# Kernel optimization log

Measured on AMD Instinct MI355X. Metric: run time of the kernel, lower is better.

The kernel has to match this reference:

```python
import jax, jax.numpy as jnp
import numpy as np

NUM_EXPERTS = 8
HIDDEN = 2048
FFN = 1376
CAPACITY_FACTOR = 1.25
SCORE_SCALE = 1.0


def setup_inputs() -> dict:
    key = jax.random.key(0)
    k = jax.random.split(key, 6)
    T = 8192
    x = jax.random.normal(k[0], (T, HIDDEN), dtype=jnp.float32)
    topK_indices = jax.random.randint(k[1], (T,), 0, NUM_EXPERTS, dtype=jnp.int64)
    topK_scores = jax.random.uniform(k[2], (T,), dtype=jnp.float32)
    s = 1.0 / np.sqrt(HIDDEN)
    w_gate = jax.random.normal(k[3], (NUM_EXPERTS, HIDDEN, FFN), dtype=jnp.float32) * s
    w_up = jax.random.normal(k[4], (NUM_EXPERTS, HIDDEN, FFN), dtype=jnp.float32) * s
    w_down = jax.random.normal(k[5], (NUM_EXPERTS, FFN, HIDDEN), dtype=jnp.float32) * (1.0 / np.sqrt(FFN))
    return {"x": x, "topK_indices": topK_indices, "topK_scores": topK_scores,
            "w_gate": w_gate, "w_up": w_up, "w_down": w_down}


def reference(x, topK_indices, topK_scores, w_gate, w_up, w_down):
    T, D = x.shape
    E = w_gate.shape[0]
    capacity = int(CAPACITY_FACTOR * T / E)  # static (depends only on shapes)
    # position of each token within its assigned expert (deterministic drop:
    # keep the first `capacity` tokens in sequence order per expert)
    oh = jax.nn.one_hot(topK_indices, E, dtype=jnp.int32)          # [T,E]
    rank = jnp.take_along_axis(jnp.cumsum(oh, axis=0) - 1,
                               topK_indices[:, None].astype(jnp.int32), axis=1)[:, 0]
    keep = rank < capacity                                          # [T]
    # dispatch into per-expert capacity buffers; dropped tokens go to dummy slot
    slot = jnp.where(keep, topK_indices.astype(jnp.int32) * capacity + rank, E * capacity)
    buf = jnp.zeros((E * capacity + 1, D), x.dtype)
    buf = buf.at[slot].set(jnp.where(keep[:, None], x, jnp.zeros_like(x)))
    xe = buf[:E * capacity].reshape(E, capacity, D)                 # [E,C,D]
    # per-expert SwiGLU MLP as grouped GEMMs
    h = jax.nn.silu(jnp.einsum('ecd,edf->ecf', xe, w_gate)) * jnp.einsum('ecd,edf->ecf', xe, w_up)
    out = jnp.einsum('ecf,efd->ecd', h, w_down).reshape(E * capacity, D)
    out = jnp.concatenate([out, jnp.zeros((1, D), out.dtype)], axis=0)
    # combine: dropped tokens -> zero (dropped_padding='zero'), gate-score fusion
    y = out[slot] * keep[:, None].astype(out.dtype)
    y = y * (topK_scores[:, None] * SCORE_SCALE)
    return y
```

## Files before the change

kernel.cpp:

```cpp
#include <hip/hip_runtime.h>
#include <hip/hip_bf16.h>
#include <cstdint>
#include <cstddef>

#define NTOK 8192
#define DH   2048
#define DF   1376
#define DFP  1408
#define NE   8
#define CAP  1280

typedef __bf16 bf16x8 __attribute__((ext_vector_type(8)));
typedef float  f32x4  __attribute__((ext_vector_type(4)));

#define BARRIER() asm volatile("s_barrier" ::: "memory")
#define WAITV0()  asm volatile("s_waitcnt vmcnt(0)" ::: "memory")
#define WAITV6()  asm volatile("s_waitcnt vmcnt(6)" ::: "memory")
#define WAITV8()  asm volatile("s_waitcnt vmcnt(8)" ::: "memory")
#define SETPRIO(n) __builtin_amdgcn_s_setprio(n)

__device__ __forceinline__ uint32_t pk2(float a, float b) {
  float2 f; f.x = a; f.y = b;
  union { __hip_bfloat162 h; uint32_t u; } cv;
  cv.h = __float22bfloat162_rn(f);
  return cv.u;
}
__device__ __forceinline__ ushort bf16bits(float a) {
  return (ushort)(pk2(a, 0.f) & 0xFFFFu);
}
__device__ __forceinline__ void gload16(const ushort* g, ushort* l) {
  __builtin_amdgcn_global_load_lds(
      (const __attribute__((address_space(1))) uint32_t*)(const void*)g,
      (__attribute__((address_space(3))) uint32_t*)(void*)l,
      16, 0, 0);
}

__global__ void routing_kernel(const int* __restrict__ idx, int* __restrict__ tok_slot,
                               int* __restrict__ tok_keep) {
  __shared__ int cnt[256][NE];
  const int t = threadIdx.x;
  for (int s = t; s < NE * CAP; s += 256) tok_slot[s] = -1;
  unsigned long long cA = 0ull, cB = 0ull;
  const int per = NTOK / 256, base = t * per;
  for (int i = 0; i < per; ++i) {
    int e = idx[base + i];
    unsigned long long inc = 1ull << ((e & 3) * 16);
    if (e < 4) cA += inc; else cB += inc;
  }
#pragma unroll
  for (int e = 0; e < 4; ++e) cnt[t][e]     = (int)((cA >> (e * 16)) & 0xFFFF);
#pragma unroll
  for (int e = 0; e < 4; ++e) cnt[t][4 + e] = (int)((cB >> (e * 16)) & 0xFFFF);
  __syncthreads();
  if (t < NE) {
    int run = 0;
    for (int i = 0; i < 256; ++i) { int c = cnt[i][t]; cnt[i][t] = run; run += c; }
  }
  __syncthreads();
  cA = 0ull; cB = 0ull;
#pragma unroll
  for (int e = 0; e < 4; ++e) cA |= (unsigned long long)(cnt[t][e] & 0xFFFF) << (e * 16);
#pragma unroll
  for (int e = 0; e < 4; ++e) cB |= (unsigned long long)(cnt[t][4 + e] & 0xFFFF) << (e * 16);
  for (int i = 0; i < per; ++i) {
    int token = base + i;
    int e = idx[token];
    int sh = (e & 3) * 16;
    int r = (int)(((e < 4 ? cA : cB) >> sh) & 0xFFFF);
    unsigned long long inc = 1ull << sh;
    if (e < 4) cA += inc; else cB += inc;
    bool keep = (r < CAP);
    tok_keep[token] = keep ? 1 : 0;
    if (keep) tok_slot[e * CAP + r] = token;
  }
}

__global__ void zero_dropped(const int* __restrict__ keep, float* __restrict__ y) {
  if (keep[blockIdx.x]) return;
  float4 z = {0.f, 0.f, 0.f, 0.f};
  float* p = y + (size_t)blockIdx.x * DH + threadIdx.x * 8;
  *(float4*)p = z;
  *(float4*)(p + 4) = z;
}

__global__ void convert_x(const float* __restrict__ x, ushort* __restrict__ xb) {
  int i = (blockIdx.x * 256 + threadIdx.x) * 8;
  float4 a = *(const float4*)(x + i);
  float4 b = *(const float4*)(x + i + 4);
  uint4 p = { pk2(a.x, a.y), pk2(a.z, a.w), pk2(b.x, b.y), pk2(b.z, b.w) };
  *(uint4*)(xb + i) = p;
}

__global__ __launch_bounds__(256) void transpose_cvt(
    const float* __restrict__ in, ushort* __restrict__ out, int K, int N) {
  __shared__ ushort T[64][72];
  const int tid = threadIdx.x;
  const int n0 = blockIdx.x * 64, k0 = blockIdx.y * 64;
  const size_t eoff_in  = (size_t)blockIdx.z * K * N;
  const size_t eoff_out = (size_t)blockIdx.z * N * K;
  const int kr = tid >> 4;
  const int nc = (tid & 15) * 4;
#pragma unroll
  for (int it = 0; it < 4; ++it) {
    int k = k0 + kr + it * 16;
    int n = n0 + nc;
    float4 v = {0.f, 0.f, 0.f, 0.f};
    if (k < K && n + 4 <= N) v = *(const float4*)(in + eoff_in + (size_t)k * N + n);
    T[nc + 0][kr + it * 16] = bf16bits(v.x);
    T[nc + 1][kr + it * 16] = bf16bits(v.y);
    T[nc + 2][kr + it * 16] = bf16bits(v.z);
    T[nc + 3][kr + it * 16] = bf16bits(v.w);
  }
  __syncthreads();
  const int nr = tid >> 2;
  const int kc = tid & 3;
#pragma unroll
  for (int it = 0; it < 2; ++it) {
    int kloc = kc * 16 + it * 8;
    int n = n0 + nr, k = k0 + kloc;
    if (n < N && k + 8 <= K)
      *(uint4*)(out + eoff_out + (size_t)n * K + k) = *(const uint4*)&T[nr][kloc];
  }
}

__global__ void pad_h(ushort* __restrict__ h) {
  int idx = blockIdx.x * 512 + threadIdx.x;
  int row = idx >> 2, q = idx & 3;
  uint4 z = {0u, 0u, 0u, 0u};
  *(uint4*)(h + (size_t)row * DFP + DF + q * 8) = z;
}

__global__ __launch_bounds__(512, 1) void gemm_gateup3(
    const ushort* __restrict__ xb, const ushort* __restrict__ wgt,
    const ushort* __restrict__ wut, const int* __restrict__ tok_slot,
    ushort* __restrict__ h)
{
  __shared__ __align__(16) char sm[131072];
  const int tid = threadIdx.x, lane = tid & 63, wid = tid >> 6;
  const int wr = wid >> 1, wc = wid & 1;
  const int l15 = lane & 15, l4 = lane >> 4;

  int wgid = (blockIdx.x & 7) * 55 + (blockIdx.x >> 3);
  const int e = wgid / 55;
  const int rem = wgid - e * 55;
  const int mt = rem / 11, nt = rem - (rem / 11) * 11;
  const int n0 = nt * 128;

  const ushort* srcA[2]; const ushort* srcBg; const ushort* srcBu;
#pragma unroll
  for (int c = 0; c < 2; ++c) {
    int o = c * 8192 + wid * 1024 + lane * 16;
    int os = o ^ (((o >> 6) & 3) << 4);
    int row = os >> 6, kb = os & 63;
    int tk = tok_slot[e * CAP + mt * 256 + row];
    if (tk < 0) tk = 0;
    srcA[c] = xb + (size_t)tk * DH + (kb >> 1);
  }
  {
    int o = wid * 1024 + lane * 16;
    int os = o ^ (((o >> 6) & 3) << 4);
    int row = os >> 6, kb = os & 63;
    int n = n0 + row; if (n > DF - 1) n = DF - 1;
    srcBg = wgt + ((size_t)e * DF + n) * DH + (kb >> 1);
    srcBu = wut + ((size_t)e * DF + n) * DH + (kb >> 1);
  }
  int aoff[4], boff[4];
#pragma unroll
  for (int i = 0; i < 4; ++i) {
    int row = wr * 64 + i * 16 + l15;
    aoff[i] = row * 64 + ((l4 * 16) ^ ((l15 & 3) << 4));
  }
#pragma unroll
  for (int j = 0; j < 4; ++j) {
    int row = wc * 64 + j * 16 + l15;
    boff[j] = row * 64 + ((l4 * 16) ^ ((l15 & 3) << 4));
  }
  const int dstw = wid * 1024;

  f32x4 accG[4][4], accU[4][4];
#pragma unroll
  for (int i = 0; i < 4; ++i)
#pragma unroll
    for (int j = 0; j < 4; ++j) {
      accG[i][j] = (f32x4){0.f, 0.f, 0.f, 0.f};
      accU[i][j] = (f32x4){0.f, 0.f, 0.f, 0.f};
    }

  const int NT = DH / 32;
#pragma unroll
  for (int t0 = 0; t0 < 3; ++t0) {
    int kk = t0 * 32;
    gload16(srcA[0] + kk, (ushort*)(sm + t0 * 16384 + dstw));
    gload16(srcA[1] + kk, (ushort*)(sm + t0 * 16384 + 8192 + dstw));
    gload16(srcBg   + kk, (ushort*)(sm + 65536 + t0 * 8192 + dstw));
    gload16(srcBu   + kk, (ushort*)(sm + 98304 + t0 * 8192 + dstw));
  }
  WAITV8();
  BARRIER();

  for (int t = 0; t < NT; ++t) {
    const int r = t & 3, w = (t + 3) & 3;
    char* Ab  = sm + r * 16384;
    char* Bgb = sm + 65536 + r * 8192;
    char* Bub = sm + 98304 + r * 8192;
    bf16x8 a[4], bg[4], bu[4];
#pragma unroll
    for (int i = 0; i < 4; ++i) a[i]  = *(const bf16x8*)(Ab + aoff[i]);
#pragma unroll
    for (int j = 0; j < 4; ++j) bg[j] = *(const bf16x8*)(Bgb + boff[j]);
#pragma unroll
    for (int j = 0; j < 4; ++j) bu[j] = *(const bf16x8*)(Bub + boff[j]);
    if (t + 3 < NT) {
      int kk = (t + 3) * 32;
      gload16(srcA[0] + kk, (ushort*)(sm + w * 16384 + dstw));
      gload16(srcA[1] + kk, (ushort*)(sm + w * 16384 + 8192 + dstw));
      gload16(srcBg   + kk, (ushort*)(sm + 65536 + w * 8192 + dstw));
      gload16(srcBu   + kk, (ushort*)(sm + 98304 + w * 8192 + dstw));
    }
    SETPRIO(1);
#pragma unroll
    for (int j = 0; j < 4; ++j)
#pragma unroll
      for (int i = 0; i < 4; ++i)
        accG[i][j] = __builtin_amdgcn_mfma_f32_16x16x32_bf16(a[i], bg[j], accG[i][j], 0, 0, 0);
#pragma unroll
    for (int j = 0; j < 4; ++j)
#pragma unroll
      for (int i = 0; i < 4; ++i)
        accU[i][j] = __builtin_amdgcn_mfma_f32_16x16x32_bf16(a[i], bu[j], accU[i][j], 0, 0, 0);
    SETPRIO(0);
    if (t >= NT - 2) { WAITV0(); } else { WAITV8(); }
    BARRIER();
  }
  const size_t rowbase = (size_t)(e * CAP + mt * 256 + wr * 64);
#pragma unroll
  for (int j = 0; j < 4; ++j) {
    int col = n0 + wc * 64 + j * 16 + l15;
    if (col < DF) {
#pragma unroll
      for (int i = 0; i < 4; ++i)
#pragma unroll
        for (int r2 = 0; r2 < 4; ++r2) {
          size_t row = rowbase + i * 16 + l4 * 4 + r2;
          float gv = accG[i][j][r2], uv = accU[i][j][r2];
          h[row * DFP + col] = bf16bits(gv / (1.f + __expf(-gv)) * uv);
        }
    }
  }
}

__global__ __launch_bounds__(512, 1) void gemm_down3(
    const ushort* __restrict__ h, const ushort* __restrict__ wdt,
    const int* __restrict__ tok_slot, const float* __restrict__ scores,
    float* __restrict__ y)
{
  __shared__ __align__(16) char sm[149504];
  int* tokc = (int*)(sm + 147456);
  float* scc = (float*)(sm + 148480);
  const int tid = threadIdx.x, lane = tid & 63, wid = tid >> 6;
  const int wr = wid >> 1, wc = wid & 1;
  const int l15 = lane & 15, l4 = lane >> 4;

  int wgid = (blockIdx.x & 7) * 80 + (blockIdx.x >> 3);
  const int e = wgid / 80;
  const int rem = wgid - e * 80;
  const int mt = rem / 16, nt = rem & 15;
  const int n0 = nt * 128;

  if (tid < 256) {
    int tk = tok_slot[e * CAP + mt * 256 + tid];
    tokc[tid] = tk;
    scc[tid] = (tk >= 0) ? scores[tk] : 0.f;
  }
  __syncthreads();

  const size_t hrow0 = (size_t)(e * CAP + mt * 256);
  const ushort* srcA[4]; const ushort* srcB[2];
#pragma unroll
  for (int c = 0; c < 4; ++c) {
    int o = c * 8192 + wid * 1024 + lane * 16;
    int os = o ^ (((o >> 7) & 7) << 4);
    int row = os >> 7, kb = os & 127;
    srcA[c] = h + (hrow0 + row) * DFP + (kb >> 1);
  }
#pragma unroll
  for (int c = 0; c < 2; ++c) {
    int o = c * 8192 + wid * 1024 + lane * 16;
    int os = o ^ (((o >> 7) & 7) << 4);
    int row = os >> 7, kb = os & 127;
    srcB[c] = wdt + ((size_t)e * DH + n0 + row) * DF + (kb >> 1);
  }
  int aoff0[4], aoff1[4], boff0[4], boff1[4];
#pragma unroll
  for (int i = 0; i < 4; ++i) {
    int row = wr * 64 + i * 16 + l15;
    int r4 = (row & 7) << 4;
    aoff0[i] = row * 128 + ((l4 * 16) ^ r4);
    aoff1[i] = row * 128 + ((l4 * 16 + 64) ^ r4);
  }
#pragma unroll
  for (int j = 0; j < 4; ++j) {
    int row = wc * 64 + j * 16 + l15;
    int r4 = (row & 7) << 4;
    boff0[j] = row * 128 + ((l4 * 16) ^ r4);
    boff1[j] = row * 128 + ((l4 * 16 + 64) ^ r4);
  }
  const int dstw = wid * 1024;

  f32x4 acc[4][4];
#pragma unroll
  for (int i = 0; i < 4; ++i)
#pragma unroll
    for (int j = 0; j < 4; ++j) acc[i][j] = (f32x4){0.f, 0.f, 0.f, 0.f};

  const int NT = DFP / 64;
#pragma unroll
  for (int t0 = 0; t0 < 2; ++t0) {
    int kk = t0 * 64;
#pragma unroll
    for (int c = 0; c < 4; ++c)
      gload16(srcA[c] + kk, (ushort*)(sm + t0 * 32768 + c * 8192 + dstw));
#pragma unroll
    for (int c = 0; c < 2; ++c)
      gload16(srcB[c] + kk, (ushort*)(sm + 98304 + t0 * 16384 + c * 8192 + dstw));
  }
  WAITV6();
  BARRIER();

  int rrot = 0, wrot = 2;
  for (int t = 0; t < NT; ++t) {
    char* Ab = sm + rrot * 32768;
    char* Bb = sm + 98304 + rrot * 16384;
    bf16x8 a0[4], a1[4], b0[4], b1[4];
#pragma unroll
    for (int i = 0; i < 4; ++i) a0[i] = *(const bf16x8*)(Ab + aoff0[i]);
#pragma unroll
    for (int j = 0; j < 4; ++j) b0[j] = *(const bf16x8*)(Bb + boff0[j]);
#pragma unroll
    for (int i = 0; i < 4; ++i) a1[i] = *(const bf16x8*)(Ab + aoff1[i]);
#pragma unroll
    for (int j = 0; j < 4; ++j) b1[j] = *(const bf16x8*)(Bb + boff1[j]);
    if (t + 2 < NT) {
      int kk = (t + 2) * 64;
#pragma unroll
      for (int c = 0; c < 4; ++c)
        gload16(srcA[c] + kk, (ushort*)(sm + wrot * 32768 + c * 8192 + dstw));
#pragma unroll
      for (int c = 0; c < 2; ++c)
        gload16(srcB[c] + kk, (ushort*)(sm + 98304 + wrot * 16384 + c * 8192 + dstw));
    }
    SETPRIO(1);
#pragma unroll
    for (int j = 0; j < 4; ++j)
#pragma unroll
      for (int i = 0; i < 4; ++i)
        acc[i][j] = __builtin_amdgcn_mfma_f32_16x16x32_bf16(a0[i], b0[j], acc[i][j], 0, 0, 0);
#pragma unroll
    for (int j = 0; j < 4; ++j)
#pragma unroll
      for (int i = 0; i < 4; ++i)
        acc[i][j] = __builtin_amdgcn_mfma_f32_16x16x32_bf16(a1[i], b1[j], acc[i][j], 0, 0, 0);
    SETPRIO(0);
    if (t >= NT - 2) { WAITV0(); } else { WAITV6(); }
    BARRIER();
    rrot = (rrot == 2) ? 0 : rrot + 1;
    wrot = (wrot == 2) ? 0 : wrot + 1;
  }
  int tkr[4][4]; float sr[4][4];
#pragma unroll
  for (int i = 0; i < 4; ++i)
#pragma unroll
    for (int r = 0; r < 4; ++r) {
      int rl = wr * 64 + i * 16 + l4 * 4 + r;
      tkr[i][r] = tokc[rl];
      sr[i][r]  = scc[rl];
    }
#pragma unroll
  for (int j = 0; j < 4; ++j) {
    int col = n0 + wc * 64 + j * 16 + l15;
#pragma unroll
    for (int i = 0; i < 4; ++i)
#pragma unroll
      for (int r = 0; r < 4; ++r)
        if (tkr[i][r] >= 0)
          y[(size_t)tkr[i][r] * DH + col] = acc[i][j][r] * sr[i][r];
  }
}

extern "C" void kernel_launch(void* const* d_in, const int* in_sizes, int n_in,
                              void* d_out, int out_size, void* d_ws, size_t ws_size,
                              hipStream_t stream) {
  const float* x   = (const float*)d_in[0];
  const int*   idx = (const int*)d_in[1];
  const float* sc  = (const float*)d_in[2];
  const float* wg  = (const float*)d_in[3];
  const float* wu  = (const float*)d_in[4];
  const float* wd  = (const float*)d_in[5];
  float* y = (float*)d_out;

  const size_t OFF_KEEP = 40960;
  const size_t OFF_H    = 73728;
  const size_t SZ_H     = (size_t)NE * CAP * DFP * 2;
  const size_t OFF_XB   = OFF_H + SZ_H;
  const size_t SZ_XB    = (size_t)NTOK * DH * 2;
  const size_t OFF_WGT  = OFF_XB + SZ_XB;
  const size_t SZ_W     = (size_t)NE * DH * DF * 2;
  const size_t OFF_WUT  = OFF_WGT + SZ_W;

  int* tok_slot = (int*)d_ws;
  int* tok_keep = (int*)((char*)d_ws + OFF_KEEP);
  ushort* hbuf = (ushort*)((char*)d_ws + OFF_H);
  ushort* xb   = (ushort*)((char*)d_ws + OFF_XB);
  ushort* wgt  = (ushort*)((char*)d_ws + OFF_WGT);
  ushort* wut  = (ushort*)((char*)d_ws + OFF_WUT);
  ushort* wdt  = wgt;

  hipLaunchKernelGGL(routing_kernel, dim3(1), dim3(256), 0, stream, idx, tok_slot, tok_keep);
  hipLaunchKernelGGL(zero_dropped, dim3(NTOK), dim3(256), 0, stream, tok_keep, y);
  hipLaunchKernelGGL(convert_x, dim3(NTOK * DH / 2048), dim3(256), 0, stream, x, xb);
  hipLaunchKernelGGL(transpose_cvt, dim3((DF + 63) / 64, DH / 64, NE), dim3(256), 0, stream,
                     wg, wgt, DH, DF);
  hipLaunchKernelGGL(transpose_cvt, dim3((DF + 63) / 64, DH / 64, NE), dim3(256), 0, stream,
                     wu, wut, DH, DF);
  hipLaunchKernelGGL(pad_h, dim3(80), dim3(512), 0, stream, hbuf);
  hipLaunchKernelGGL(gemm_gateup3, dim3(440), dim3(512), 0, stream,
                     xb, wgt, wut, tok_slot, hbuf);
  hipLaunchKernelGGL(transpose_cvt, dim3(DH / 64, (DF + 63) / 64, NE), dim3(256), 0, stream,
                     wd, wdt, DF, DH);
  hipLaunchKernelGGL(gemm_down3, dim3(640), dim3(512), 0, stream,
                     hbuf, wdt, tok_slot, sc, y);
}
```

Baseline: 350.0 us.

## Use row-paired LDS swizzle and 4-stage K=32 pipeline in down GEMM

Both GEMMs switch to a new LDS layout that packs two 32-element K rows into each 128-byte line with an XOR swizzle, aimed at reducing LDS bank conflicts on the MFMA fragment reads. The down-projection kernel changes from a 3-buffer K=64 pipeline to a 4-buffer K=32 pipeline prefetching three tiles ahead, which shrinks its shared memory footprint. The vmcnt waits at the pipeline tail are graduated instead of draining everything early. Smaller K steps mean more barriers per unit of work in the down GEMM.

New measurement: 356.0 us. No clear change (+1.7%).

```diff
diff --git a/kernel.cpp b/kernel.cpp
--- a/kernel.cpp
+++ b/kernel.cpp
@@ -14,9 +14,7 @@
 typedef float  f32x4  __attribute__((ext_vector_type(4)));
 
 #define BARRIER() asm volatile("s_barrier" ::: "memory")
-#define WAITV0()  asm volatile("s_waitcnt vmcnt(0)" ::: "memory")
-#define WAITV6()  asm volatile("s_waitcnt vmcnt(6)" ::: "memory")
-#define WAITV8()  asm volatile("s_waitcnt vmcnt(8)" ::: "memory")
+#define WAITV(n)  asm volatile("s_waitcnt vmcnt(" #n ")" ::: "memory")
 #define SETPRIO(n) __builtin_amdgcn_s_setprio(n)
 
 __device__ __forceinline__ uint32_t pk2(float a, float b) {
@@ -33,6 +31,16 @@
       (const __attribute__((address_space(1))) uint32_t*)(const void*)g,
       (__attribute__((address_space(3))) uint32_t*)(void*)l,
       16, 0, 0);
+}
+
+__device__ __forceinline__ void rp_src(int o, int& row, int& ko) {
+  int p = o >> 7;
+  int g = ((o >> 4) & 7) ^ (p & 7);
+  row = p * 2 + (g >> 2);
+  ko  = (g & 3) * 8;
+}
+__device__ __forceinline__ int rp_off(int row, int l4) {
+  return ((row >> 1) << 7) + (((((row & 1) << 2) + l4) ^ ((row >> 1) & 7)) << 4);
 }
 
 __global__ void routing_kernel(const int* __restrict__ idx, int* __restrict__ tok_slot,
@@ -150,31 +158,23 @@
 #pragma unroll
   for (int c = 0; c < 2; ++c) {
     int o = c * 8192 + wid * 1024 + lane * 16;
-    int os = o ^ (((o >> 6) & 3) << 4);
-    int row = os >> 6, kb = os & 63;
+    int row, ko; rp_src(o, row, ko);
     int tk = tok_slot[e * CAP + mt * 256 + row];
     if (tk < 0) tk = 0;
-    srcA[c] = xb + (size_t)tk * DH + (kb >> 1);
+    srcA[c] = xb + (size_t)tk * DH + ko;
   }
   {
     int o = wid * 1024 + lane * 16;
-    int os = o ^ (((o >> 6) & 3) << 4);
-    int row = os >> 6, kb = os & 63;
+    int row, ko; rp_src(o, row, ko);
     int n = n0 + row; if (n > DF - 1) n = DF - 1;
-    srcBg = wgt + ((size_t)e * DF + n) * DH + (kb >> 1);
-    srcBu = wut + ((size_t)e * DF + n) * DH + (kb >> 1);
+    srcBg = wgt + ((size_t)e * DF + n) * DH + ko;
+    srcBu = wut + ((size_t)e * DF + n) * DH + ko;
   }
   int aoff[4], boff[4];
 #pragma unroll
-  for (int i = 0; i < 4; ++i) {
-    int row = wr * 64 + i * 16 + l15;
-    aoff[i] = row * 64 + ((l4 * 16) ^ ((l15 & 3) << 4));
-  }
-#pragma unroll
-  for (int j = 0; j < 4; ++j) {
-    int row = wc * 64 + j * 16 + l15;
-    boff[j] = row * 64 + ((l4 * 16) ^ ((l15 & 3) << 4));
-  }
+  for (int i = 0; i < 4; ++i) aoff[i] = rp_off(wr * 64 + i * 16 + l15, l4);
+#pragma unroll
+  for (int j = 0; j < 4; ++j) boff[j] = rp_off(wc * 64 + j * 16 + l15, l4);
   const int dstw = wid * 1024;
 
   f32x4 accG[4][4], accU[4][4];
@@ -195,7 +195,7 @@
     gload16(srcBg   + kk, (ushort*)(sm + 65536 + t0 * 8192 + dstw));
     gload16(srcBu   + kk, (ushort*)(sm + 98304 + t0 * 8192 + dstw));
   }
-  WAITV8();
+  WAITV(8);
   BARRIER();
 
   for (int t = 0; t < NT; ++t) {
@@ -229,7 +229,9 @@
       for (int i = 0; i < 4; ++i)
         accU[i][j] = __builtin_amdgcn_mfma_f32_16x16x32_bf16(a[i], bu[j], accU[i][j], 0, 0, 0);
     SETPRIO(0);
-    if (t >= NT - 2) { WAITV0(); } else { WAITV8(); }
+    if (t + 3 < NT)      { WAITV(8); }
+    else if (t + 2 < NT) { WAITV(4); }
+    else if (t + 1 < NT) { WAITV(0); }
     BARRIER();
   }
   const size_t rowbase = (size_t)(e * CAP + mt * 256 + wr * 64);
@@ -254,9 +256,9 @@
     const int* __restrict__ tok_slot, const float* __restrict__ scores,
     float* __restrict__ y)
 {
-  __shared__ __align__(16) char sm[149504];
-  int* tokc = (int*)(sm + 147456);
-  float* scc = (float*)(sm + 148480);
+  __shared__ __align__(16) char sm[100352];
+  int* tokc = (int*)(sm + 98304);
+  float* scc = (float*)(sm + 99328);
   const int tid = threadIdx.x, lane = tid & 63, wid = tid >> 6;
   const int wr = wid >> 1, wc = wid & 1;
   const int l15 = lane & 15, l4 = lane >> 4;
@@ -275,36 +277,23 @@
   __syncthreads();
 
   const size_t hrow0 = (size_t)(e * CAP + mt * 256);
-  const ushort* srcA[4]; const ushort* srcB[2];
-#pragma unroll
-  for (int c = 0; c < 4; ++c) {
-    int o = c * 8192 + wid * 1024 + lane * 16;
-    int os = o ^ (((o >> 7) & 7) << 4);
-    int row = os >> 7, kb = os & 127;
-    srcA[c] = h + (hrow0 + row) * DFP + (kb >> 1);
-  }
+  const ushort* srcA[2]; const ushort* srcB;
 #pragma unroll
   for (int c = 0; c < 2; ++c) {
     int o = c * 8192 + wid * 1024 + lane * 16;
-    int os = o ^ (((o >> 7) & 7) << 4);
-    int row = os >> 7, kb = os & 127;
-    srcB[c] = wdt + ((size_t)e * DH + n0 + row) * DF + (kb >> 1);
-  }
-  int aoff0[4], aoff1[4], boff0[4], boff1[4];
-#pragma unroll
-  for (int i = 0; i < 4; ++i) {
-    int row = wr * 64 + i * 16 + l15;
-    int r4 = (row & 7) << 4;
-    aoff0[i] = row * 128 + ((l4 * 16) ^ r4);
-    aoff1[i] = row * 128 + ((l4 * 16 + 64) ^ r4);
-  }
-#pragma unroll
-  for (int j = 0; j < 4; ++j) {
-    int row = wc * 64 + j * 16 + l15;
-    int r4 = (row & 7) << 4;
-    boff0[j] = row * 128 + ((l4 * 16) ^ r4);
-    boff1[j] = row * 128 + ((l4 * 16 + 64) ^ r4);
-  }
+    int row, ko; rp_src(o, row, ko);
+    srcA[c] = h + (hrow0 + row) * DFP + ko;
+  }
+  {
+    int o = wid * 1024 + lane * 16;
+    int row, ko; rp_src(o, row, ko);
+    srcB = wdt + ((size_t)e * DH + n0 + row) * DF + ko;
+  }
+  int aoff[4], boff[4];
+#pragma unroll
+  for (int i = 0; i < 4; ++i) aoff[i] = rp_off(wr * 64 + i * 16 + l15, l4);
+#pragma unroll
+  for (int j = 0; j < 4; ++j) boff[j] = rp_off(wc * 64 + j * 16 + l15, l4);
   const int dstw = wid * 1024;
 
   f32x4 acc[4][4];
@@ -313,58 +302,43 @@
 #pragma unroll
     for (int j = 0; j < 4; ++j) acc[i][j] = (f32x4){0.f, 0.f, 0.f, 0.f};
 
-  const int NT = DFP / 64;
-#pragma unroll
-  for (int t0 = 0; t0 < 2; ++t0) {
-    int kk = t0 * 64;
-#pragma unroll
-    for (int c = 0; c < 4; ++c)
-      gload16(srcA[c] + kk, (ushort*)(sm + t0 * 32768 + c * 8192 + dstw));
-#pragma unroll
-    for (int c = 0; c < 2; ++c)
-      gload16(srcB[c] + kk, (ushort*)(sm + 98304 + t0 * 16384 + c * 8192 + dstw));
-  }
-  WAITV6();
+  const int NT = DFP / 32;
+#pragma unroll
+  for (int t0 = 0; t0 < 3; ++t0) {
+    int kk = t0 * 32;
+    gload16(srcA[0] + kk, (ushort*)(sm + t0 * 16384 + dstw));
+    gload16(srcA[1] + kk, (ushort*)(sm + t0 * 16384 + 8192 + dstw));
+    gload16(srcB    + kk, (ushort*)(sm + 65536 + t0 * 8192 + dstw));
+  }
+  WAITV(6);
   BARRIER();
 
-  int rrot = 0, wrot = 2;
   for (int t = 0; t < NT; ++t) {
-    char* Ab = sm + rrot * 32768;
-    char* Bb = sm + 98304 + rrot * 16384;
-    bf16x8 a0[4], a1[4], b0[4], b1[4];
-#pragma unroll
-    for (int i = 0; i < 4; ++i) a0[i] = *(const bf16x8*)(Ab + aoff0[i]);
-#pragma unroll
-    for (int j = 0; j < 4; ++j) b0[j] = *(const bf16x8*)(Bb + boff0[j]);
-#pragma unroll
-    for (int i = 0; i < 4; ++i) a1[i] = *(const bf16x8*)(Ab + aoff1[i]);
-#pragma unroll
-    for (int j = 0; j < 4; ++j) b1[j] = *(const bf16x8*)(Bb + boff1[j]);
-    if (t + 2 < NT) {
-      int kk = (t + 2) * 64;
-#pragma unroll
-      for (int c = 0; c < 4; ++c)
-        gload16(srcA[c] + kk, (ushort*)(sm + wrot * 32768 + c * 8192 + dstw));
-#pragma unroll
-      for (int c = 0; c < 2; ++c)
-        gload16(srcB[c] + kk, (ushort*)(sm + 98304 + wrot * 16384 + c * 8192 + dstw));
+    const int r = t & 3, w = (t + 3) & 3;
+    char* Ab = sm + r * 16384;
+    char* Bb = sm + 65536 + r * 8192;
+    bf16x8 a[4], b[4];
+#pragma unroll
+    for (int i = 0; i < 4; ++i) a[i] = *(const bf16x8*)(Ab + aoff[i]);
+#pragma unroll
+    for (int j = 0; j < 4; ++j) b[j] = *(const bf16x8*)(Bb + boff[j]);
+    if (t + 3 < NT) {
+      int kk = (t + 3) * 32;
+      gload16(srcA[0] + kk, (ushort*)(sm + w * 16384 + dstw));
+      gload16(srcA[1] + kk, (ushort*)(sm + w * 16384 + 8192 + dstw));
+      gload16(srcB    + kk, (ushort*)(sm + 65536 + w * 8192 + dstw));
     }
     SETPRIO(1);
 #pragma unroll
     for (int j = 0; j < 4; ++j)
 #pragma unroll
       for (int i = 0; i < 4; ++i)
-        acc[i][j] = __builtin_amdgcn_mfma_f32_16x16x32_bf16(a0[i], b0[j], acc[i][j], 0, 0, 0);
-#pragma unroll
-    for (int j = 0; j < 4; ++j)
-#pragma unroll
-      for (int i = 0; i < 4; ++i)
-        acc[i][j] = __builtin_amdgcn_mfma_f32_16x16x32_bf16(a1[i], b1[j], acc[i][j], 0, 0, 0);
+        acc[i][j] = __builtin_amdgcn_mfma_f32_16x16x32_bf16(a[i], b[j], acc[i][j], 0, 0, 0);
     SETPRIO(0);
-    if (t >= NT - 2) { WAITV0(); } else { WAITV6(); }
+    if (t + 3 < NT)      { WAITV(6); }
+    else if (t + 2 < NT) { WAITV(3); }
+    else if (t + 1 < NT) { WAITV(0); }
     BARRIER();
-    rrot = (rrot == 2) ? 0 : rrot + 1;
-    wrot = (wrot == 2) ? 0 : wrot + 1;
   }
   int tkr[4][4]; float sr[4][4];
 #pragma unroll
```
